# Performance work log

Measured on AMD Instinct MI355X. Metric: run time of the kernel, lower is better.

Reference implementation:

```python
import jax, jax.numpy as jnp
import numpy as np

N = 100000   # nodes
D = 64       # padded neighbor-list width (avg degree)
F = 256      # in_channels
H = 256      # hidden_channels
E = 131072   # number of target edges
OUT = 1      # out_channels


def _linear_params(key, fin, fout):
    k1, k2 = jax.random.split(key)
    s = 1.0 / np.sqrt(fin)
    w = jax.random.uniform(k1, (fin, fout), jnp.float32, -s, s)
    b = jax.random.uniform(k2, (fout,), jnp.float32, -s, s)
    return w, b


def setup_inputs() -> dict:
    key = jax.random.key(0)
    ks = jax.random.split(key, 12)
    x = jax.random.normal(ks[0], (N, F), jnp.float32)
    # sorted padded neighbor lists: row i -> D neighbor ids (sorted, as in the
    # bit-packed sorted-element representation the torch code intersects)
    neighbors = jnp.sort(jax.random.randint(ks[1], (N, D), 0, N), axis=1).astype(jnp.int32)
    tar_ei = jax.random.randint(ks[2], (2, E), 0, N).astype(jnp.int32)
    cn_w1, cn_b1 = _linear_params(ks[3], 1, H)
    cn_w2, cn_b2 = _linear_params(ks[4], H, H)
    cn_w3, cn_b3 = _linear_params(ks[5], H, H)
    ij_w1, ij_b1 = _linear_params(ks[6], F, H)
    ij_w2, ij_b2 = _linear_params(ks[7], H, H)
    lin_w1, lin_b1 = _linear_params(ks[8], H, H)
    lin_w2, lin_b2 = _linear_params(ks[9], H, OUT)
    beta = jnp.ones((1,), jnp.float32)
    return dict(x=x, neighbors=neighbors, tar_ei=tar_ei, beta=beta,
                cn_w1=cn_w1, cn_b1=cn_b1, cn_w2=cn_w2, cn_b2=cn_b2,
                cn_w3=cn_w3, cn_b3=cn_b3,
                ij_w1=ij_w1, ij_b1=ij_b1, ij_w2=ij_w2, ij_b2=ij_b2,
                lin_w1=lin_w1, lin_b1=lin_b1, lin_w2=lin_w2, lin_b2=lin_b2)


def reference(x, neighbors, tar_ei, beta,
              cn_w1, cn_b1, cn_w2, cn_b2, cn_w3, cn_b3,
              ij_w1, ij_b1, ij_w2, ij_b2,
              lin_w1, lin_b1, lin_w2, lin_b2):
    src, dst = tar_ei[0], tar_ei[1]
    xi = x[src]                       # [E, F] irregular gather
    xj = x[dst]                       # [E, F]

    # adjoverlap / spmoverlap_: per edge, |N(i) ∩ N(j)| via sorted-set
    # intersection; cn.sum(dim=-1) with fill value 1.0 -> CN count.
    ni = neighbors[src]               # [E, D]
    nj = neighbors[dst]               # [E, D]
    matches = ni[:, :, None] == nj[:, None, :]          # [E, D, D]
    xcn = jnp.sum(matches, axis=(1, 2)).astype(jnp.float32)[:, None]  # [E, 1]

    # xcnlin: Linear(1,H) -> ReLU -> Linear(H,H) -> ReLU -> Linear(H,H)
    h = jax.nn.relu(xcn @ cn_w1 + cn_b1)
    h = jax.nn.relu(h @ cn_w2 + cn_b2)
    xcn_feat = h @ cn_w3 + cn_b3                         # [E, H]

    # xijlin: Linear(F,H) -> ReLU -> Linear(H,H)
    g = jax.nn.relu((xi * xj) @ ij_w1 + ij_b1)
    xij = g @ ij_w2 + ij_b2                              # [E, H]

    # lin: Linear(H,H) -> ReLU -> Linear(H,OUT)
    z = jax.nn.relu((xcn_feat * beta + xij) @ lin_w1 + lin_b1)
    out = z @ lin_w2 + lin_b2                            # [E, OUT]
    return out
```

## Files before the change

### kernel.cpp

```cpp
#include <hip/hip_runtime.h>
#include <hip/hip_bf16.h>
#include <stdint.h>

#define EE 131072
#define DDEG 64

typedef __bf16 bf16_t;
typedef bf16_t bf16x8 __attribute__((ext_vector_type(8)));
typedef float floatx4 __attribute__((ext_vector_type(4)));

#define SWZ(row, k) (((row) << 8) + ((k) ^ (((row) & 7) << 3)))

__global__ __launch_bounds__(256)
void prep_kernel(const float* __restrict__ x, bf16_t* __restrict__ xb,
                 const int* __restrict__ tar, const int* __restrict__ nbr,
                 int* __restrict__ xcnbuf,
                 const float* __restrict__ ij_w1, bf16_t* __restrict__ Wt1,
                 const float* __restrict__ w2, const float* __restrict__ lw1,
                 bf16_t* __restrict__ Mt,
                 const float* __restrict__ b2, const float* __restrict__ lb1,
                 float* __restrict__ cvec,
                 const float* __restrict__ cw1, const float* __restrict__ cb1,
                 const float* __restrict__ cw2, const float* __restrict__ cb2,
                 const float* __restrict__ cw3, const float* __restrict__ cb3,
                 const float* __restrict__ beta, float* __restrict__ T2) {
    __shared__ __align__(16) char arena[33792];
    const int bid = blockIdx.x;
    const int t = threadIdx.x;

    if (bid >= 3136) {
        size_t base = (size_t)(bid - 3136) * 4096 + (size_t)t * 16;
        float4 a0 = *(const float4*)(x + base);
        float4 a1 = *(const float4*)(x + base + 4);
        float4 a2 = *(const float4*)(x + base + 8);
        float4 a3 = *(const float4*)(x + base + 12);
        bf16x8 o0, o1;
        o0[0] = (bf16_t)a0.x; o0[1] = (bf16_t)a0.y; o0[2] = (bf16_t)a0.z; o0[3] = (bf16_t)a0.w;
        o0[4] = (bf16_t)a1.x; o0[5] = (bf16_t)a1.y; o0[6] = (bf16_t)a1.z; o0[7] = (bf16_t)a1.w;
        o1[0] = (bf16_t)a2.x; o1[1] = (bf16_t)a2.y; o1[2] = (bf16_t)a2.z; o1[3] = (bf16_t)a2.w;
        o1[4] = (bf16_t)a3.x; o1[5] = (bf16_t)a3.y; o1[6] = (bf16_t)a3.z; o1[7] = (bf16_t)a3.w;
        *(bf16x8*)(xb + base)     = o0;
        *(bf16x8*)(xb + base + 8) = o1;
        return;
    }

    if (bid < 2048) {
        const int lane = t & 63;
        const int wcn  = t >> 6;
        const int e0   = bid * 64 + wcn * 16;
        int va[16], vb[16];
        #pragma unroll
        for (int i = 0; i < 16; ++i) {
            int e = e0 + i;
            int s = __builtin_amdgcn_readfirstlane(tar[e]);
            int d = __builtin_amdgcn_readfirstlane(tar[EE + e]);
            va[i] = nbr[(size_t)s * DDEG + lane];
            vb[i] = nbr[(size_t)d * DDEG + lane];
        }
        #pragma unroll
        for (int p = 0; p < 8; ++p) {
            int cpk = 0;
            #pragma unroll
            for (int h = 0; h < 2; ++h) {
                int i = p * 2 + h;
                int lo = 0, hi = 0;
                #pragma unroll
                for (int st = 32; st; st >>= 1) {
                    int bl = __shfl(vb[i], lo + st - 1, 64);
                    int bh = __shfl(vb[i], hi + st - 1, 64);
                    lo += (bl < va[i]) ? st : 0;
                    hi += (bh <= va[i]) ? st : 0;
                }
                int b63 = __shfl(vb[i], 63, 64);
                lo += (b63 < va[i]) ? 1 : 0;
                hi += (b63 <= va[i]) ? 1 : 0;
                cpk += (hi - lo) << (16 * h);
            }
            #pragma unroll
            for (int off = 32; off; off >>= 1) cpk += __shfl_xor(cpk, off, 64);
            if (lane == 0) {
                int c0 = cpk & 0xffff, c1 = (int)((unsigned)cpk >> 16);
                xcnbuf[e0 + p * 2]     = c0 < 511 ? c0 : 511;
                xcnbuf[e0 + p * 2 + 1] = c1 < 511 ? c1 : 511;
            }
        }
        return;
    }

    const int b2id = bid - 2048;
    if (b2id < 64) {
        float (*tile)[33] = (float (*)[33])arena;
        int bx = b2id & 7, by = b2id >> 3;
        int tx = t & 31, ty = t >> 5;
        #pragma unroll
        for (int r = 0; r < 32; r += 8)
            tile[ty + r][tx] = ij_w1[(by * 32 + ty + r) * 256 + bx * 32 + tx];
        __syncthreads();
        #pragma unroll
        for (int r = 0; r < 32; r += 8)
            Wt1[(bx * 32 + ty + r) * 256 + by * 32 + tx] = (bf16_t)tile[tx][ty + r];
    } else if (b2id < 320) {
        float (*S)[33] = (float (*)[33])arena;
        int b = b2id - 64;
        int cc = t & 31, abase = t >> 5;
        float acc = 0.f;
        for (int c0 = 0; c0 < 256; c0 += 32) {
            __syncthreads();
            #pragma unroll
            for (int r = 0; r < 32; ++r) {
                int a = r * 8 + abase;
                S[a][cc] = w2[a * 256 + c0 + cc];
            }
            __syncthreads();
            #pragma unroll 8
            for (int c2 = 0; c2 < 32; ++c2) {
                float wv = lw1[(c0 + c2) * 256 + b];
                acc += S[t][c2] * wv;
            }
        }
        Mt[(size_t)b * 256 + t] = (bf16_t)acc;
    } else if (b2id < 576) {
        float* red = (float*)arena;
        int b = b2id - 320;
        red[t] = b2[t] * lw1[t * 256 + b];
        __syncthreads();
        for (int s = 128; s > 0; s >>= 1) {
            if (t < s) red[t] += red[t + s];
            __syncthreads();
        }
        if (t == 0) cvec[b] = red[0] + lb1[b];
    } else {
        float* t1 = (float*)arena;
        float* t2 = (float*)(arena + 1024);
        float* t3 = (float*)(arena + 2048);
        int v = b2id - 576;
        float fv = (float)v;
        t1[t] = fmaxf(fv * cw1[t] + cb1[t], 0.f);
        __syncthreads();
        float s = cb2[t];
        for (int k = 0; k < 256; ++k) s += t1[k] * cw2[k * 256 + t];
        t2[t] = fmaxf(s, 0.f);
        __syncthreads();
        s = cb3[t];
        for (int k = 0; k < 256; ++k) s += t2[k] * cw3[k * 256 + t];
        t3[t] = s * beta[0];
        __syncthreads();
        s = 0.f;
        for (int k = 0; k < 256; ++k) s += t3[k] * lw1[k * 256 + t];
        T2[(size_t)v * 256 + t] = s;
    }
}

__global__ __launch_bounds__(256, 3)
void fused_kernel(const bf16_t* __restrict__ xb, const int* __restrict__ tar,
                  const bf16_t* __restrict__ Wt1, const float* __restrict__ b1,
                  const bf16_t* __restrict__ Mt, const float* __restrict__ cvec,
                  const float* __restrict__ T2, const int* __restrict__ xcnbuf,
                  const float* __restrict__ w2, const float* __restrict__ b2s,
                  float* __restrict__ out) {
    __shared__ __align__(16) bf16_t X[64 * 256];

    const int tid  = threadIdx.x;
    const int lane = tid & 63;
    const int wc   = tid >> 6;
    const int quad = lane >> 4;
    const int l16  = lane & 15;
    const int e0   = blockIdx.x * 64;

    {
        const int srow   = tid >> 2;
        const int skbase = (tid & 3) * 8;
        int e = e0 + srow;
        const bf16_t* xi = xb + (size_t)tar[e] * 256 + skbase;
        const bf16_t* xj = xb + (size_t)tar[EE + e] * 256 + skbase;
        #pragma unroll
        for (int c = 0; c < 2; ++c) {
            bf16x8 ui[4], vj[4];
            #pragma unroll
            for (int k2 = 0; k2 < 4; ++k2) {
                ui[k2] = *(const bf16x8*)(xi + (c * 4 + k2) * 32);
                vj[k2] = *(const bf16x8*)(xj + (c * 4 + k2) * 32);
            }
            #pragma unroll
            for (int k2 = 0; k2 < 4; ++k2) {
                bf16x8 p;
                #pragma unroll
                for (int m = 0; m < 8; ++m)
                    p[m] = (bf16_t)((float)ui[k2][m] * (float)vj[k2][m]);
                *(bf16x8*)&X[SWZ(srow, (c * 4 + k2) * 32 + skbase)] = p;
            }
        }
    }

    floatx4 acc[4][4];
    #pragma unroll
    for (int i = 0; i < 4; ++i)
        #pragma unroll
        for (int j = 0; j < 4; ++j)
            acc[i][j] = (floatx4){0.f, 0.f, 0.f, 0.f};

    __syncthreads();

    #pragma unroll 2
    for (int kc = 0; kc < 8; ++kc) {
        const int k0 = kc * 32 + quad * 8;
        bf16x8 af[4], bfr[4];
        #pragma unroll
        for (int j = 0; j < 4; ++j)
            bfr[j] = *(const bf16x8*)(Wt1 + (size_t)(wc * 64 + j * 16 + l16) * 256 + k0);
        #pragma unroll
        for (int i = 0; i < 4; ++i)
            af[i] = *(const bf16x8*)(&X[SWZ(i * 16 + l16, k0)]);
        #pragma unroll
        for (int i = 0; i < 4; ++i)
            #pragma unroll
            for (int j = 0; j < 4; ++j)
                acc[i][j] = __builtin_amdgcn_mfma_f32_16x16x32_bf16(
                                af[i], bfr[j], acc[i][j], 0, 0, 0);
    }

    __syncthreads();

    #pragma unroll
    for (int j = 0; j < 4; ++j) {
        int col  = wc * 64 + j * 16 + l16;
        float bv = b1[col];
        #pragma unroll
        for (int i = 0; i < 4; ++i)
            #pragma unroll
            for (int r = 0; r < 4; ++r) {
                int row = i * 16 + quad * 4 + r;
                X[SWZ(row, col)] = (bf16_t)fmaxf(acc[i][j][r] + bv, 0.f);
            }
    }
    #pragma unroll
    for (int i = 0; i < 4; ++i)
        #pragma unroll
        for (int j = 0; j < 4; ++j)
            acc[i][j] = (floatx4){0.f, 0.f, 0.f, 0.f};

    __syncthreads();

    #pragma unroll 2
    for (int kc = 0; kc < 8; ++kc) {
        const int k0 = kc * 32 + quad * 8;
        bf16x8 af[4], bfr[4];
        #pragma unroll
        for (int j = 0; j < 4; ++j)
            bfr[j] = *(const bf16x8*)(Mt + (size_t)(wc * 64 + j * 16 + l16) * 256 + k0);
        #pragma unroll
        for (int i = 0; i < 4; ++i)
            af[i] = *(const bf16x8*)(&X[SWZ(i * 16 + l16, k0)]);
        #pragma unroll
        for (int i = 0; i < 4; ++i)
            #pragma unroll
            for (int j = 0; j < 4; ++j)
                acc[i][j] = __builtin_amdgcn_mfma_f32_16x16x32_bf16(
                                af[i], bfr[j], acc[i][j], 0, 0, 0);
    }

    int xv[16];
    #pragma unroll
    for (int i = 0; i < 4; ++i)
        #pragma unroll
        for (int r = 0; r < 4; ++r)
            xv[i * 4 + r] = xcnbuf[e0 + i * 16 + quad * 4 + r];

    float pr[16];
    #pragma unroll
    for (int t = 0; t < 16; ++t) pr[t] = 0.f;
    #pragma unroll
    for (int j = 0; j < 4; ++j) {
        int col  = wc * 64 + j * 16 + l16;
        float cv = cvec[col];
        float wv = w2[col];
        #pragma unroll
        for (int i = 0; i < 4; ++i)
            #pragma unroll
            for (int r = 0; r < 4; ++r) {
                float t2v = T2[(size_t)xv[i * 4 + r] * 256 + col];
                float v = fmaxf(acc[i][j][r] + cv + t2v, 0.f);
                pr[i * 4 + r] += v * wv;
            }
    }
    #pragma unroll
    for (int off = 1; off < 16; off <<= 1)
        #pragma unroll
        for (int t = 0; t < 16; ++t)
            pr[t] += __shfl_xor(pr[t], off, 64);

    __syncthreads();
    float* red = (float*)X;
    if (l16 == 0) {
        #pragma unroll
        for (int i = 0; i < 4; ++i)
            #pragma unroll
            for (int r = 0; r < 4; ++r)
                red[wc * 64 + i * 16 + quad * 4 + r] = pr[i * 4 + r];
    }
    __syncthreads();
    if (tid < 64)
        out[e0 + tid] = red[tid] + red[64 + tid] + red[128 + tid]
                      + red[192 + tid] + b2s[0];
}

extern "C" void kernel_launch(void* const* d_in, const int* in_sizes, int n_in,
                              void* d_out, int out_size, void* d_ws, size_t ws_size,
                              hipStream_t stream) {
    const float* x      = (const float*)d_in[0];
    const int*   nbr    = (const int*)  d_in[1];
    const int*   tar    = (const int*)  d_in[2];
    const float* beta   = (const float*)d_in[3];
    const float* cn_w1  = (const float*)d_in[4];
    const float* cn_b1  = (const float*)d_in[5];
    const float* cn_w2  = (const float*)d_in[6];
    const float* cn_b2  = (const float*)d_in[7];
    const float* cn_w3  = (const float*)d_in[8];
    const float* cn_b3  = (const float*)d_in[9];
    const float* ij_w1  = (const float*)d_in[10];
    const float* ij_b1  = (const float*)d_in[11];
    const float* ij_w2  = (const float*)d_in[12];
    const float* ij_b2  = (const float*)d_in[13];
    const float* lin_w1 = (const float*)d_in[14];
    const float* lin_b1 = (const float*)d_in[15];
    const float* lin_w2 = (const float*)d_in[16];
    const float* lin_b2 = (const float*)d_in[17];

    char* ws = (char*)d_ws;
    float*  T2     = (float*) (ws + 0);
    int*    xcnbuf = (int*)   (ws + 524288);
    bf16_t* Wt1    = (bf16_t*)(ws + 1048576);
    bf16_t* Mt     = (bf16_t*)(ws + 1179648);
    float*  cvec   = (float*) (ws + 1310720);
    bf16_t* xb     = (bf16_t*)(ws + 1312768);

    prep_kernel<<<3136 + 6250, 256, 0, stream>>>(
        x, xb, tar, nbr, xcnbuf,
        ij_w1, Wt1, ij_w2, lin_w1, Mt,
        ij_b2, lin_b1, cvec,
        cn_w1, cn_b1, cn_w2, cn_b2, cn_w3, cn_b3, beta, T2);
    fused_kernel<<<EE / 64, 256, 0, stream>>>(xb, tar, Wt1, ij_b1, Mt, cvec,
                                              T2, xcnbuf, lin_w2, lin_b2,
                                              (float*)d_out);
}
```

Measured before the change: 318.8 us.

## Split fused kernel tile across 8 waves with 2x4 wave grid

```diff
diff --git a/kernel.cpp b/kernel.cpp
--- a/kernel.cpp
+++ b/kernel.cpp
@@ -151,7 +151,7 @@
     }
 }
 
-__global__ __launch_bounds__(256, 3)
+__global__ __launch_bounds__(512, 4)
 void fused_kernel(const bf16_t* __restrict__ xb, const int* __restrict__ tar,
                   const bf16_t* __restrict__ Wt1, const float* __restrict__ b1,
                   const bf16_t* __restrict__ Mt, const float* __restrict__ cvec,
@@ -162,39 +162,38 @@
 
     const int tid  = threadIdx.x;
     const int lane = tid & 63;
-    const int wc   = tid >> 6;
+    const int wave = tid >> 6;
+    const int wr   = wave >> 2;
+    const int wcN  = wave & 3;
     const int quad = lane >> 4;
     const int l16  = lane & 15;
     const int e0   = blockIdx.x * 64;
 
     {
-        const int srow   = tid >> 2;
-        const int skbase = (tid & 3) * 8;
+        const int srow   = tid >> 3;
+        const int skbase = (tid & 7) * 8;
         int e = e0 + srow;
         const bf16_t* xi = xb + (size_t)tar[e] * 256 + skbase;
         const bf16_t* xj = xb + (size_t)tar[EE + e] * 256 + skbase;
-        #pragma unroll
-        for (int c = 0; c < 2; ++c) {
-            bf16x8 ui[4], vj[4];
-            #pragma unroll
-            for (int k2 = 0; k2 < 4; ++k2) {
-                ui[k2] = *(const bf16x8*)(xi + (c * 4 + k2) * 32);
-                vj[k2] = *(const bf16x8*)(xj + (c * 4 + k2) * 32);
-            }
-            #pragma unroll
-            for (int k2 = 0; k2 < 4; ++k2) {
-                bf16x8 p;
-                #pragma unroll
-                for (int m = 0; m < 8; ++m)
-                    p[m] = (bf16_t)((float)ui[k2][m] * (float)vj[k2][m]);
-                *(bf16x8*)&X[SWZ(srow, (c * 4 + k2) * 32 + skbase)] = p;
-            }
-        }
-    }
-
-    floatx4 acc[4][4];
-    #pragma unroll
-    for (int i = 0; i < 4; ++i)
+        bf16x8 ui[4], vj[4];
+        #pragma unroll
+        for (int kc = 0; kc < 4; ++kc) {
+            ui[kc] = *(const bf16x8*)(xi + kc * 64);
+            vj[kc] = *(const bf16x8*)(xj + kc * 64);
+        }
+        #pragma unroll
+        for (int kc = 0; kc < 4; ++kc) {
+            bf16x8 p;
+            #pragma unroll
+            for (int m = 0; m < 8; ++m)
+                p[m] = (bf16_t)((float)ui[kc][m] * (float)vj[kc][m]);
+            *(bf16x8*)&X[SWZ(srow, kc * 64 + skbase)] = p;
+        }
+    }
+
+    floatx4 acc[2][4];
+    #pragma unroll
+    for (int i = 0; i < 2; ++i)
         #pragma unroll
         for (int j = 0; j < 4; ++j)
             acc[i][j] = (floatx4){0.f, 0.f, 0.f, 0.f};
@@ -204,15 +203,15 @@
     #pragma unroll 2
     for (int kc = 0; kc < 8; ++kc) {
         const int k0 = kc * 32 + quad * 8;
-        bf16x8 af[4], bfr[4];
+        bf16x8 af[2], bfr[4];
         #pragma unroll
         for (int j = 0; j < 4; ++j)
-            bfr[j] = *(const bf16x8*)(Wt1 + (size_t)(wc * 64 + j * 16 + l16) * 256 + k0);
-        #pragma unroll
-        for (int i = 0; i < 4; ++i)
-            af[i] = *(const bf16x8*)(&X[SWZ(i * 16 + l16, k0)]);
-        #pragma unroll
-        for (int i = 0; i < 4; ++i)
+            bfr[j] = *(const bf16x8*)(Wt1 + (size_t)(wcN * 64 + j * 16 + l16) * 256 + k0);
+        #pragma unroll
+        for (int i = 0; i < 2; ++i)
+            af[i] = *(const bf16x8*)(&X[SWZ(wr * 32 + i * 16 + l16, k0)]);
+        #pragma unroll
+        for (int i = 0; i < 2; ++i)
             #pragma unroll
             for (int j = 0; j < 4; ++j)
                 acc[i][j] = __builtin_amdgcn_mfma_f32_16x16x32_bf16(
@@ -223,18 +222,18 @@
 
     #pragma unroll
     for (int j = 0; j < 4; ++j) {
-        int col  = wc * 64 + j * 16 + l16;
+        int col  = wcN * 64 + j * 16 + l16;
         float bv = b1[col];
         #pragma unroll
-        for (int i = 0; i < 4; ++i)
+        for (int i = 0; i < 2; ++i)
             #pragma unroll
             for (int r = 0; r < 4; ++r) {
-                int row = i * 16 + quad * 4 + r;
+                int row = wr * 32 + i * 16 + quad * 4 + r;
                 X[SWZ(row, col)] = (bf16_t)fmaxf(acc[i][j][r] + bv, 0.f);
             }
     }
     #pragma unroll
-    for (int i = 0; i < 4; ++i)
+    for (int i = 0; i < 2; ++i)
         #pragma unroll
         for (int j = 0; j < 4; ++j)
             acc[i][j] = (floatx4){0.f, 0.f, 0.f, 0.f};
@@ -244,38 +243,38 @@
     #pragma unroll 2
     for (int kc = 0; kc < 8; ++kc) {
         const int k0 = kc * 32 + quad * 8;
-        bf16x8 af[4], bfr[4];
+        bf16x8 af[2], bfr[4];
         #pragma unroll
         for (int j = 0; j < 4; ++j)
-            bfr[j] = *(const bf16x8*)(Mt + (size_t)(wc * 64 + j * 16 + l16) * 256 + k0);
-        #pragma unroll
-        for (int i = 0; i < 4; ++i)
-            af[i] = *(const bf16x8*)(&X[SWZ(i * 16 + l16, k0)]);
-        #pragma unroll
-        for (int i = 0; i < 4; ++i)
+            bfr[j] = *(const bf16x8*)(Mt + (size_t)(wcN * 64 + j * 16 + l16) * 256 + k0);
+        #pragma unroll
+        for (int i = 0; i < 2; ++i)
+            af[i] = *(const bf16x8*)(&X[SWZ(wr * 32 + i * 16 + l16, k0)]);
+        #pragma unroll
+        for (int i = 0; i < 2; ++i)
             #pragma unroll
             for (int j = 0; j < 4; ++j)
                 acc[i][j] = __builtin_amdgcn_mfma_f32_16x16x32_bf16(
                                 af[i], bfr[j], acc[i][j], 0, 0, 0);
     }
 
-    int xv[16];
-    #pragma unroll
-    for (int i = 0; i < 4; ++i)
+    int xv[8];
+    #pragma unroll
+    for (int i = 0; i < 2; ++i)
         #pragma unroll
         for (int r = 0; r < 4; ++r)
-            xv[i * 4 + r] = xcnbuf[e0 + i * 16 + quad * 4 + r];
-
-    float pr[16];
-    #pragma unroll
-    for (int t = 0; t < 16; ++t) pr[t] = 0.f;
+            xv[i * 4 + r] = xcnbuf[e0 + wr * 32 + i * 16 + quad * 4 + r];
+
+    float pr[8];
+    #pragma unroll
+    for (int t = 0; t < 8; ++t) pr[t] = 0.f;
     #pragma unroll
     for (int j = 0; j < 4; ++j) {
-        int col  = wc * 64 + j * 16 + l16;
+        int col  = wcN * 64 + j * 16 + l16;
         float cv = cvec[col];
         float wv = w2[col];
         #pragma unroll
-        for (int i = 0; i < 4; ++i)
+        for (int i = 0; i < 2; ++i)
             #pragma unroll
             for (int r = 0; r < 4; ++r) {
                 float t2v = T2[(size_t)xv[i * 4 + r] * 256 + col];
@@ -286,17 +285,17 @@
     #pragma unroll
     for (int off = 1; off < 16; off <<= 1)
         #pragma unroll
-        for (int t = 0; t < 16; ++t)
+        for (int t = 0; t < 8; ++t)
             pr[t] += __shfl_xor(pr[t], off, 64);
 
     __syncthreads();
     float* red = (float*)X;
     if (l16 == 0) {
         #pragma unroll
-        for (int i = 0; i < 4; ++i)
+        for (int i = 0; i < 2; ++i)
             #pragma unroll
             for (int r = 0; r < 4; ++r)
-                red[wc * 64 + i * 16 + quad * 4 + r] = pr[i * 4 + r];
+                red[wcN * 64 + wr * 32 + i * 16 + quad * 4 + r] = pr[i * 4 + r];
     }
     __syncthreads();
     if (tid < 64)
@@ -339,7 +338,7 @@
         ij_w1, Wt1, ij_w2, lin_w1, Mt,
         ij_b2, lin_b1, cvec,
         cn_w1, cn_b1, cn_w2, cn_b2, cn_w3, cn_b3, beta, T2);
-    fused_kernel<<<EE / 64, 256, 0, stream>>>(xb, tar, Wt1, ij_b1, Mt, cvec,
+    fused_kernel<<<EE / 64, 512, 0, stream>>>(xb, tar, Wt1, ij_b1, Mt, cvec,
                                               T2, xcnbuf, lin_w2, lin_b2,
                                               (float*)d_out);
 }
```

After: 355.8 us. +11.6%, slower.
